# Optimization experiments

Hardware: AMD Instinct MI355X
Metric: run time of the kernel (lower is better)

## Reference

```python
import jax, jax.numpy as jnp
import numpy as np

B, S, D = 4, 2048, 1024
E, H, K = 8, 2048, 2


def setup_inputs() -> dict:
    key = jax.random.key(0)
    k_x, k_g, k1, k2, k3 = jax.random.split(key, 5)
    x = jax.random.normal(k_x, (B, S, D), dtype=jnp.float32)
    # nn.Linear weight layout is [out, in]
    Wg = jax.random.normal(k_g, (E, D), dtype=jnp.float32) * 0.02   # gate
    W1 = jax.random.normal(k1, (E, H, D), dtype=jnp.float32) * 0.02  # fc1, stacked over experts
    W2 = jax.random.normal(k2, (E, H, D), dtype=jnp.float32) * 0.02  # fc2
    W3 = jax.random.normal(k3, (E, D, H), dtype=jnp.float32) * 0.02  # fc3
    return {"x": x, "Wg": Wg, "W1": W1, "W2": W2, "W3": W3}


def reference(x, Wg, W1, W2, W3):
    # gating
    scores = jnp.einsum("bsd,ed->bse", x, Wg)                 # [B,S,E]
    topk_scores, topk_idx = jax.lax.top_k(scores, K)          # [B,S,K]
    topk_probs = jax.nn.softmax(topk_scores, axis=-1)         # [B,S,K]
    # scatter top-k probs back to a dense [B,S,E] gate (indices are distinct per token)
    gating = jnp.sum(jax.nn.one_hot(topk_idx, E, dtype=x.dtype) * topk_probs[..., None], axis=-2)  # [B,S,E]
    # dense compute-all-experts SwiGLU (faithful to source)
    h1 = jnp.einsum("bsd,ehd->bseh", x, W1)                   # [B,S,E,H]
    h2 = jnp.einsum("bsd,ehd->bseh", x, W2)
    hidden = jax.nn.silu(h1) * h2
    expert_out = jnp.einsum("bseh,edh->bsed", hidden, W3)     # [B,S,E,D]
    y = jnp.einsum("bse,bsed->bsd", gating, expert_out)       # weighted combine
    return y
```

## Files before the change

kernel.cpp:

```cpp
#include <hip/hip_runtime.h>
#include <hip/hip_bf16.h>
#include <cstdint>
#include <cstddef>

typedef unsigned short u16;
typedef uint32_t u32;
typedef __attribute__((ext_vector_type(4))) float f32x4;
typedef __attribute__((ext_vector_type(8))) short bf16x8;

#define NTOK 8192
#define DIM  1024
#define HID  2048
#define NEXP 8
#define MAXT1 72
#define MAXT2 136

#define GLD16(g, l) __builtin_amdgcn_global_load_lds( \
    (const __attribute__((address_space(1))) void*)(g), \
    (__attribute__((address_space(3))) void*)(l), 16, 0, 0)

#define WAITV(n) asm volatile("s_waitcnt vmcnt(" #n ")" ::: "memory")

__device__ __forceinline__ u16 f2bf(float f) {
  __hip_bfloat16 h = __float2bfloat16(f);
  return __builtin_bit_cast(u16, h);
}
__device__ __forceinline__ float bf2f(short s) {
  u32 u = ((u32)(u16)s) << 16;
  return __builtin_bit_cast(float, u);
}

__device__ __forceinline__ const bf16x8* lds_frag(const u16* base, int row, int chunk) {
  return (const bf16x8*)(base + row * 64 + ((chunk ^ (row & 7)) << 3));
}

__global__ __launch_bounds__(256) void convert3_kernel(
    const float4* __restrict__ s0, const float4* __restrict__ s1,
    const float4* __restrict__ s2, ushort4* __restrict__ d0,
    ushort4* __restrict__ d1, ushort4* __restrict__ d2) {
  const int n4 = 1 << 22;
  int stride = gridDim.x * blockDim.x;
  for (int i = blockIdx.x * blockDim.x + threadIdx.x; i < 3 * n4; i += stride) {
    int t = i >> 22, off = i & (n4 - 1);
    const float4* s = (t == 0) ? s0 : (t == 1) ? s1 : s2;
    ushort4* d      = (t == 0) ? d0 : (t == 1) ? d1 : d2;
    float4 v = s[off];
    ushort4 o;
    o.x = f2bf(v.x); o.y = f2bf(v.y); o.z = f2bf(v.z); o.w = f2bf(v.w);
    d[off] = o;
  }
}

__global__ __launch_bounds__(256) void gating_kernel(
    const float4* __restrict__ x4, const float4* __restrict__ Wg4,
    int* __restrict__ gate_idx, float* __restrict__ gate_prob,
    u16* __restrict__ Xb) {
  int tid = threadIdx.x, w = tid >> 6, l = tid & 63;
  int t = blockIdx.x * 4 + w;

  float4 xv[4];
#pragma unroll
  for (int j = 0; j < 4; ++j)
    xv[j] = x4[(size_t)t * 256 + l + 64 * j];

  float acc[NEXP];
#pragma unroll
  for (int e = 0; e < NEXP; ++e) acc[e] = 0.f;
#pragma unroll
  for (int e = 0; e < NEXP; ++e)
#pragma unroll
    for (int j = 0; j < 4; ++j) {
      float4 wv = Wg4[e * 256 + l + 64 * j];
      acc[e] += xv[j].x * wv.x + xv[j].y * wv.y + xv[j].z * wv.z + xv[j].w * wv.w;
    }

#pragma unroll
  for (int j = 0; j < 4; ++j) {
    ushort4 o;
    o.x = f2bf(xv[j].x); o.y = f2bf(xv[j].y);
    o.z = f2bf(xv[j].z); o.w = f2bf(xv[j].w);
    *(ushort4*)&Xb[(size_t)t * DIM + (l + 64 * j) * 4] = o;
  }

#pragma unroll
  for (int off = 32; off >= 1; off >>= 1)
#pragma unroll
    for (int e = 0; e < NEXP; ++e)
      acc[e] += __shfl_xor(acc[e], off);

  if (l == 0) {
    float best = -1e30f, sec = -1e30f;
    int bi = 0, si = 0;
#pragma unroll
    for (int e = 0; e < NEXP; ++e) {
      float s = acc[e];
      if (s > best)      { sec = best; si = bi; best = s; bi = e; }
      else if (s > sec)  { sec = s; si = e; }
    }
    float e1  = __expf(sec - best);
    float inv = 1.f / (1.f + e1);
    gate_idx[t * 2]      = bi;
    gate_idx[t * 2 + 1]  = si;
    gate_prob[t * 2]     = inv;
    gate_prob[t * 2 + 1] = e1 * inv;
  }
}

__global__ __launch_bounds__(256) void hist_kernel(
    const int* __restrict__ gate_idx, int* __restrict__ counts) {
  __shared__ int h[NEXP];
  int tid = threadIdx.x;
  if (tid < NEXP) h[tid] = 0;
  __syncthreads();
  int i = blockIdx.x * 256 + tid;
  atomicAdd(&h[gate_idx[i]], 1);
  __syncthreads();
  if (tid < NEXP) atomicAdd(&counts[tid], h[tid]);
}

__global__ void scan_kernel(const int* __restrict__ counts,
                            int* __restrict__ offs, int* __restrict__ cursors,
                            int* __restrict__ tileE1, int* __restrict__ tileRow1,
                            int* __restrict__ nt1,
                            int* __restrict__ tileE2, int* __restrict__ tileRow2,
                            int* __restrict__ nt2) {
  if (threadIdx.x == 0 && blockIdx.x == 0) {
    int s = 0;
    for (int e = 0; e < NEXP; ++e) { offs[e] = s; cursors[e] = s; s += counts[e]; }
    int n1 = 0, n2 = 0;
    for (int e = 0; e < NEXP; ++e) {
      for (int r = 0; r < counts[e]; r += 256) { tileE1[n1] = e; tileRow1[n1] = r; ++n1; }
      for (int r = 0; r < counts[e]; r += 128) { tileE2[n2] = e; tileRow2[n2] = r; ++n2; }
    }
    *nt1 = n1; *nt2 = n2;
  }
}

__global__ __launch_bounds__(256) void scatter_kernel(
    const int* __restrict__ gate_idx, int* __restrict__ cursors,
    int* __restrict__ list, int* __restrict__ pos_of) {
  __shared__ int lc[NEXP];
  __shared__ int lbase[NEXP];
  int tid = threadIdx.x;
  if (tid < NEXP) lc[tid] = 0;
  __syncthreads();
  int i = blockIdx.x * 256 + tid;
  int e = gate_idx[i];
  int lp = atomicAdd(&lc[e], 1);
  __syncthreads();
  if (tid < NEXP) lbase[tid] = atomicAdd(&cursors[tid], lc[tid]);
  __syncthreads();
  int pos = lbase[e] + lp;
  list[pos] = i;
  pos_of[i] = pos;
}

__global__ __launch_bounds__(512, 2) void gemm1_kernel(
    const u16* __restrict__ Xb, const u16* __restrict__ W1b,
    const u16* __restrict__ W2b, const int* __restrict__ list,
    const int* __restrict__ offs, const int* __restrict__ counts,
    const int* __restrict__ tileE, const int* __restrict__ tileRow,
    const int* __restrict__ n_tiles, u16* __restrict__ hidden) {
  int flat = blockIdx.x + MAXT1 * blockIdx.y;
  int nf = (flat & 7) * (MAXT1 * (HID / 128) / 8) + (flat >> 3);
  int bx = nf >> 4;
  int tn = nf & 15;
  if (bx >= *n_tiles) return;
  int e = tileE[bx], row0 = tileRow[bx];
  int n_e = counts[e], off_e = offs[e];
  __shared__ u16 As[2][256 * 64];
  __shared__ u16 B1s[2][128 * 64];
  __shared__ u16 B2s[2][128 * 64];
  int tid = threadIdx.x, w = tid >> 6, l = tid & 63;
  const u16* W1e = W1b + (size_t)e * HID * DIM;
  const u16* W2e = W2b + (size_t)e * HID * DIM;

  int schunk = ((l & 7) ^ (l >> 3)) * 8;
  u32 offA[4];
#pragma unroll
  for (int j = 0; j < 4; ++j) {
    int r = w * 32 + j * 8 + (l >> 3);
    int idx = row0 + r;
    int entry = list[off_e + (idx < n_e ? idx : 0)];
    offA[j] = (u32)(entry >> 1) * DIM + schunk;
  }
  u32 offB[2];
#pragma unroll
  for (int j = 0; j < 2; ++j) {
    int r = w * 16 + j * 8 + (l >> 3);
    offB[j] = (u32)(tn * 128 + r) * DIM + schunk;
  }

#define STAGE1(buf, kt) do { u32 kof_ = (u32)(kt) * 64;                        \
    _Pragma("unroll")                                                          \
    for (int j = 0; j < 4; ++j) GLD16(Xb + offA[j] + kof_, &As[buf][w * 2048 + j * 512]); \
    _Pragma("unroll")                                                          \
    for (int j = 0; j < 2; ++j) {                                              \
      GLD16(W1e + offB[j] + kof_, &B1s[buf][w * 1024 + j * 512]);              \
      GLD16(W2e + offB[j] + kof_, &B2s[buf][w * 1024 + j * 512]);              \
    } } while (0)

  f32x4 acc1[4][4], acc2[4][4];
#pragma unroll
  for (int mi = 0; mi < 4; ++mi)
#pragma unroll
    for (int ni = 0; ni < 4; ++ni) {
      acc1[mi][ni] = (f32x4){0.f, 0.f, 0.f, 0.f};
      acc2[mi][ni] = (f32x4){0.f, 0.f, 0.f, 0.f};
    }
  int wm = w >> 1, wn = w & 1;

  STAGE1(0, 0);
  STAGE1(1, 1);
  for (int kt = 0; kt < DIM / 64; ++kt) {
    if (kt < DIM / 64 - 1) { WAITV(8); } else { WAITV(0); }
    __builtin_amdgcn_s_barrier();
    int cur = kt & 1;
    const u16* Ab  = As[cur];
    const u16* B1b = B1s[cur];
    const u16* B2b = B2s[cur];
#pragma unroll
    for (int ks = 0; ks < 2; ++ks) {
      bf16x8 a[4], b1[4], b2[4];
#pragma unroll
      for (int mi = 0; mi < 4; ++mi)
        a[mi] = *lds_frag(Ab, wm * 64 + mi * 16 + (l & 15), ks * 4 + (l >> 4));
#pragma unroll
      for (int ni = 0; ni < 4; ++ni) {
        b1[ni] = *lds_frag(B1b, wn * 64 + ni * 16 + (l & 15), ks * 4 + (l >> 4));
        b2[ni] = *lds_frag(B2b, wn * 64 + ni * 16 + (l & 15), ks * 4 + (l >> 4));
      }
#pragma unroll
      for (int mi = 0; mi < 4; ++mi)
#pragma unroll
        for (int ni = 0; ni < 4; ++ni) {
          acc1[mi][ni] = __builtin_amdgcn_mfma_f32_16x16x32_bf16(a[mi], b1[ni], acc1[mi][ni], 0, 0, 0);
          acc2[mi][ni] = __builtin_amdgcn_mfma_f32_16x16x32_bf16(a[mi], b2[ni], acc2[mi][ni], 0, 0, 0);
        }
    }
    asm volatile("" ::: "memory");
    __builtin_amdgcn_s_barrier();
    if (kt + 2 < DIM / 64) STAGE1(cur, kt + 2);
  }

#pragma unroll
  for (int mi = 0; mi < 4; ++mi) {
#pragma unroll
    for (int i = 0; i < 4; ++i) {
      int m_loc = wm * 64 + mi * 16 + (l >> 4) * 4 + i;
      int idx = row0 + m_loc;
      if (idx < n_e) {
        size_t pos = (size_t)(off_e + idx);
#pragma unroll
        for (int ni = 0; ni < 4; ++ni) {
          int h_loc = tn * 128 + wn * 64 + ni * 16 + (l & 15);
          float h1 = acc1[mi][ni][i];
          float h2 = acc2[mi][ni][i];
          float hv = h1 / (1.f + __expf(-h1)) * h2;
          hidden[pos * HID + h_loc] = f2bf(hv);
        }
      }
    }
  }
#undef STAGE1
}

__global__ __launch_bounds__(256, 2) void gemm2_kernel(
    const u16* __restrict__ hidden, const u16* __restrict__ W3b,
    const int* __restrict__ offs, const int* __restrict__ counts,
    const int* __restrict__ tileE, const int* __restrict__ tileRow,
    const int* __restrict__ n_tiles, u16* __restrict__ eout) {
  int flat = blockIdx.x + MAXT2 * blockIdx.y;
  int nf = (flat & 7) * (MAXT2 * (DIM / 128) / 8) + (flat >> 3);
  int bx = nf >> 3;
  int tn = nf & 7;
  if (bx >= *n_tiles) return;
  int e = tileE[bx], row0 = tileRow[bx];
  int n_e = counts[e], off_e = offs[e];
  __shared__ u16 As[2][128 * 64];
  __shared__ u16 Bs[2][128 * 64];
  int tid = threadIdx.x, w = tid >> 6, l = tid & 63;
  const u16* W3e = W3b + (size_t)e * DIM * HID;

  int schunk = ((l & 7) ^ (l >> 3)) * 8;
  u32 offA[4], offB[4];
#pragma unroll
  for (int j = 0; j < 4; ++j) {
    int r = w * 32 + j * 8 + (l >> 3);
    int idx = row0 + r;
    int pos = off_e + (idx < n_e ? idx : 0);
    offA[j] = (u32)pos * HID + schunk;
    offB[j] = (u32)(tn * 128 + r) * HID + schunk;
  }

#define STAGE2(buf, kt) do { u32 kof_ = (u32)(kt) * 64;                        \
    _Pragma("unroll")                                                          \
    for (int j = 0; j < 4; ++j) {                                              \
      GLD16(hidden + offA[j] + kof_, &As[buf][w * 2048 + j * 512]);            \
      GLD16(W3e    + offB[j] + kof_, &Bs[buf][w * 2048 + j * 512]);            \
    } } while (0)

  f32x4 acc[4][4];
#pragma unroll
  for (int mi = 0; mi < 4; ++mi)
#pragma unroll
    for (int ni = 0; ni < 4; ++ni) acc[mi][ni] = (f32x4){0.f, 0.f, 0.f, 0.f};
  int wm = w >> 1, wn = w & 1;

  STAGE2(0, 0);
  STAGE2(1, 1);
  for (int kt = 0; kt < HID / 64; ++kt) {
    if (kt < HID / 64 - 1) { WAITV(8); } else { WAITV(0); }
    __builtin_amdgcn_s_barrier();
    int cur = kt & 1;
    const u16* Ab = As[cur];
    const u16* Bb = Bs[cur];
#pragma unroll
    for (int ks = 0; ks < 2; ++ks) {
      bf16x8 a[4], b[4];
#pragma unroll
      for (int mi = 0; mi < 4; ++mi)
        a[mi] = *lds_frag(Ab, wm * 64 + mi * 16 + (l & 15), ks * 4 + (l >> 4));
#pragma unroll
      for (int ni = 0; ni < 4; ++ni)
        b[ni] = *lds_frag(Bb, wn * 64 + ni * 16 + (l & 15), ks * 4 + (l >> 4));
#pragma unroll
      for (int mi = 0; mi < 4; ++mi)
#pragma unroll
        for (int ni = 0; ni < 4; ++ni)
          acc[mi][ni] = __builtin_amdgcn_mfma_f32_16x16x32_bf16(a[mi], b[ni], acc[mi][ni], 0, 0, 0);
    }
    asm volatile("" ::: "memory");
    __builtin_amdgcn_s_barrier();
    if (kt + 2 < HID / 64) STAGE2(cur, kt + 2);
  }

#pragma unroll
  for (int mi = 0; mi < 4; ++mi) {
#pragma unroll
    for (int i = 0; i < 4; ++i) {
      int m_loc = wm * 64 + mi * 16 + (l >> 4) * 4 + i;
      int idx = row0 + m_loc;
      if (idx < n_e) {
        size_t pos = (size_t)(off_e + idx);
#pragma unroll
        for (int ni = 0; ni < 4; ++ni) {
          int d_loc = tn * 128 + wn * 64 + ni * 16 + (l & 15);
          eout[pos * DIM + d_loc] = f2bf(acc[mi][ni][i]);
        }
      }
    }
  }
#undef STAGE2
}

__global__ __launch_bounds__(256) void combine_kernel(
    const u16* __restrict__ eout, const int* __restrict__ pos_of,
    const float* __restrict__ gate_prob, float* __restrict__ out) {
  int gid = blockIdx.x * 256 + threadIdx.x;
  int t = gid >> 7, dq = (gid & 127) * 8;
  int p0 = pos_of[t * 2], p1 = pos_of[t * 2 + 1];
  float w0 = gate_prob[t * 2], w1 = gate_prob[t * 2 + 1];
  bf16x8 e0 = *(const bf16x8*)&eout[(size_t)p0 * DIM + dq];
  bf16x8 e1 = *(const bf16x8*)&eout[(size_t)p1 * DIM + dq];
  float4 o0, o1;
  o0.x = w0 * bf2f(e0[0]) + w1 * bf2f(e1[0]);
  o0.y = w0 * bf2f(e0[1]) + w1 * bf2f(e1[1]);
  o0.z = w0 * bf2f(e0[2]) + w1 * bf2f(e1[2]);
  o0.w = w0 * bf2f(e0[3]) + w1 * bf2f(e1[3]);
  o1.x = w0 * bf2f(e0[4]) + w1 * bf2f(e1[4]);
  o1.y = w0 * bf2f(e0[5]) + w1 * bf2f(e1[5]);
  o1.z = w0 * bf2f(e0[6]) + w1 * bf2f(e1[6]);
  o1.w = w0 * bf2f(e0[7]) + w1 * bf2f(e1[7]);
  float4* op = (float4*)&out[(size_t)t * DIM + dq];
  op[0] = o0; op[1] = o1;
}

extern "C" void kernel_launch(void* const* d_in, const int* in_sizes, int n_in,
                              void* d_out, int out_size, void* d_ws, size_t ws_size,
                              hipStream_t stream) {
  const float* x  = (const float*)d_in[0];
  const float* Wg = (const float*)d_in[1];
  const float* W1 = (const float*)d_in[2];
  const float* W2 = (const float*)d_in[3];
  const float* W3 = (const float*)d_in[4];
  float* out = (float*)d_out;

  char* wsb = (char*)d_ws;
  int*   counts    = (int*)(wsb + 0);
  int*   cursors   = (int*)(wsb + 64);
  int*   offs      = (int*)(wsb + 128);
  int*   nt1       = (int*)(wsb + 192);
  int*   nt2       = (int*)(wsb + 196);
  int*   tileE1    = (int*)(wsb + 512);
  int*   tileRow1  = (int*)(wsb + 1024);
  int*   tileE2    = (int*)(wsb + 1536);
  int*   tileRow2  = (int*)(wsb + 2560);
  int*   gate_idx  = (int*)(wsb + 4096);
  float* gate_prob = (float*)(wsb + 4096 + 65536);
  int*   pos_of    = (int*)(wsb + 4096 + 2 * 65536);
  int*   list      = (int*)(wsb + 4096 + 3 * 65536);
  u16* Xb     = (u16*)(wsb + (1 << 20));
  u16* W1b    = Xb  + (size_t)NTOK * DIM;
  u16* W2b    = W1b + (size_t)NEXP * HID * DIM;
  u16* W3b    = W2b + (size_t)NEXP * HID * DIM;
  u16* hidden = W3b + (size_t)NEXP * DIM * HID;
  u16* eout   = W1b;

  hipMemsetAsync(wsb, 0, 256, stream);

  convert3_kernel<<<4096, 256, 0, stream>>>(
      (const float4*)W1, (const float4*)W2, (const float4*)W3,
      (ushort4*)W1b, (ushort4*)W2b, (ushort4*)W3b);

  gating_kernel<<<NTOK / 4, 256, 0, stream>>>(
      (const float4*)x, (const float4*)Wg, gate_idx, gate_prob, Xb);
  hist_kernel<<<NTOK * 2 / 256, 256, 0, stream>>>(gate_idx, counts);
  scan_kernel<<<1, 64, 0, stream>>>(counts, offs, cursors,
                                    tileE1, tileRow1, nt1, tileE2, tileRow2, nt2);
  scatter_kernel<<<NTOK * 2 / 256, 256, 0, stream>>>(gate_idx, cursors, list, pos_of);

  gemm1_kernel<<<dim3(MAXT1, HID / 128), 512, 0, stream>>>(
      Xb, W1b, W2b, list, offs, counts, tileE1, tileRow1, nt1, hidden);
  gemm2_kernel<<<dim3(MAXT2, DIM / 128), 256, 0, stream>>>(
      hidden, W3b, offs, counts, tileE2, tileRow2, nt2, eout);
  combine_kernel<<<NTOK * 128 / 256, 256, 0, stream>>>(eout, pos_of, gate_prob, out);
}
```

Baseline: 360.6 us.

## Load gemm1 A fragments directly from global memory instead of staging in LDS

The gathered token activations for the first grouped GEMM are now read straight from global memory into registers per wave, instead of being staged through a double-buffered LDS tile. This drops 64 KB of LDS for A and the associated LDS reads, which may help occupancy and LDS bandwidth. In exchange each wave pair (same wm) redundantly reads the same A rows from global/L2. These global loads are issued synchronously inside the k-loop without prefetch, so their latency may be exposed before the MFMAs.

```diff
diff --git a/kernel.cpp b/kernel.cpp
--- a/kernel.cpp
+++ b/kernel.cpp
@@ -168,22 +168,23 @@
   if (bx >= *n_tiles) return;
   int e = tileE[bx], row0 = tileRow[bx];
   int n_e = counts[e], off_e = offs[e];
-  __shared__ u16 As[2][256 * 64];
   __shared__ u16 B1s[2][128 * 64];
   __shared__ u16 B2s[2][128 * 64];
   int tid = threadIdx.x, w = tid >> 6, l = tid & 63;
   const u16* W1e = W1b + (size_t)e * HID * DIM;
   const u16* W2e = W2b + (size_t)e * HID * DIM;
 
+  int wm = w >> 1, wn = w & 1;
+
+  u32 aoff[4];
+#pragma unroll
+  for (int mi = 0; mi < 4; ++mi) {
+    int idx = row0 + wm * 64 + mi * 16 + (l & 15);
+    int entry = list[off_e + (idx < n_e ? idx : 0)];
+    aoff[mi] = (u32)(entry >> 1) * DIM + (l >> 4) * 8;
+  }
+
   int schunk = ((l & 7) ^ (l >> 3)) * 8;
-  u32 offA[4];
-#pragma unroll
-  for (int j = 0; j < 4; ++j) {
-    int r = w * 32 + j * 8 + (l >> 3);
-    int idx = row0 + r;
-    int entry = list[off_e + (idx < n_e ? idx : 0)];
-    offA[j] = (u32)(entry >> 1) * DIM + schunk;
-  }
   u32 offB[2];
 #pragma unroll
   for (int j = 0; j < 2; ++j) {
@@ -191,9 +192,7 @@
     offB[j] = (u32)(tn * 128 + r) * DIM + schunk;
   }
 
-#define STAGE1(buf, kt) do { u32 kof_ = (u32)(kt) * 64;                        \
-    _Pragma("unroll")                                                          \
-    for (int j = 0; j < 4; ++j) GLD16(Xb + offA[j] + kof_, &As[buf][w * 2048 + j * 512]); \
+#define STAGEB(buf, kt) do { u32 kof_ = (u32)(kt) * 64;                        \
     _Pragma("unroll")                                                          \
     for (int j = 0; j < 2; ++j) {                                              \
       GLD16(W1e + offB[j] + kof_, &B1s[buf][w * 1024 + j * 512]);              \
@@ -208,23 +207,27 @@
       acc1[mi][ni] = (f32x4){0.f, 0.f, 0.f, 0.f};
       acc2[mi][ni] = (f32x4){0.f, 0.f, 0.f, 0.f};
     }
-  int wm = w >> 1, wn = w & 1;
-
-  STAGE1(0, 0);
-  STAGE1(1, 1);
-  for (int kt = 0; kt < DIM / 64; ++kt) {
-    if (kt < DIM / 64 - 1) { WAITV(8); } else { WAITV(0); }
+
+  const int NKT = DIM / 64;
+  STAGEB(0, 0);
+  STAGEB(1, 1);
+  for (int kt = 0; kt < NKT; ++kt) {
+    if (kt < NKT - 1) { WAITV(4); } else { WAITV(0); }
     __builtin_amdgcn_s_barrier();
     int cur = kt & 1;
-    const u16* Ab  = As[cur];
     const u16* B1b = B1s[cur];
     const u16* B2b = B2s[cur];
+
+    bf16x8 a[4][2];
+#pragma unroll
+    for (int mi = 0; mi < 4; ++mi)
+#pragma unroll
+      for (int ks = 0; ks < 2; ++ks)
+        a[mi][ks] = *(const bf16x8*)(Xb + aoff[mi] + (u32)kt * 64 + ks * 32);
+
 #pragma unroll
     for (int ks = 0; ks < 2; ++ks) {
-      bf16x8 a[4], b1[4], b2[4];
-#pragma unroll
-      for (int mi = 0; mi < 4; ++mi)
-        a[mi] = *lds_frag(Ab, wm * 64 + mi * 16 + (l & 15), ks * 4 + (l >> 4));
+      bf16x8 b1[4], b2[4];
 #pragma unroll
       for (int ni = 0; ni < 4; ++ni) {
         b1[ni] = *lds_frag(B1b, wn * 64 + ni * 16 + (l & 15), ks * 4 + (l >> 4));
@@ -234,13 +237,13 @@
       for (int mi = 0; mi < 4; ++mi)
 #pragma unroll
         for (int ni = 0; ni < 4; ++ni) {
-          acc1[mi][ni] = __builtin_amdgcn_mfma_f32_16x16x32_bf16(a[mi], b1[ni], acc1[mi][ni], 0, 0, 0);
-          acc2[mi][ni] = __builtin_amdgcn_mfma_f32_16x16x32_bf16(a[mi], b2[ni], acc2[mi][ni], 0, 0, 0);
+          acc1[mi][ni] = __builtin_amdgcn_mfma_f32_16x16x32_bf16(a[mi][ks], b1[ni], acc1[mi][ni], 0, 0, 0);
+          acc2[mi][ni] = __builtin_amdgcn_mfma_f32_16x16x32_bf16(a[mi][ks], b2[ni], acc2[mi][ni], 0, 0, 0);
         }
     }
     asm volatile("" ::: "memory");
     __builtin_amdgcn_s_barrier();
-    if (kt + 2 < DIM / 64) STAGE1(cur, kt + 2);
+    if (kt + 2 < NKT) STAGEB(cur, kt + 2);
   }
 
 #pragma unroll
@@ -262,7 +265,7 @@
       }
     }
   }
-#undef STAGE1
+#undef STAGEB
 }
 
 __global__ __launch_bounds__(256, 2) void gemm2_kernel(
```

After: 465.5 us. 1.29x slower.
